# Optimization experiments

Hardware: AMD Instinct MI355X
Metric: run time of the kernel (lower is better)

The kernel has to match this reference:

```python
import jax, jax.numpy as jnp
import numpy as np

NEG_INF = -1000000000.0
B, S, E, H = 2, 2048, 1024, 16
HD = E // H


def setup_inputs() -> dict:
    key = jax.random.key(0)
    ks = jax.random.split(key, 5)
    sd = 1.0 / np.sqrt(E)
    return {
        "x": jax.random.normal(ks[0], (B, S, E), dtype=jnp.float32),
        "Wqkv": jax.random.normal(ks[1], (3 * E, E), dtype=jnp.float32) * sd,
        "bqkv": jax.random.normal(ks[2], (3 * E,), dtype=jnp.float32) * sd,
        "Wout": jax.random.normal(ks[3], (E, E), dtype=jnp.float32) * sd,
        "bout": jax.random.normal(ks[4], (E,), dtype=jnp.float32) * sd,
    }


def reference(x, Wqkv, bqkv, Wout, bout):
    # qkv projection (torch Linear: x @ W.T + b)
    qkv = x @ Wqkv.T + bqkv                      # [B, S, 3E]
    qkv = qkv.reshape(B, S, H, 3 * HD).transpose(0, 2, 1, 3)  # [B, H, S, 3*hd]
    q, k, v = jnp.split(qkv, 3, axis=-1)          # each [B, H, S, hd]
    scaled = jnp.einsum('bhqd,bhkd->bhqk', q, k) / jnp.sqrt(jnp.float32(HD))
    # faithful to source: mask = tril(ones) * NEG_INF (lower triangle incl. diagonal gets -1e9)
    mask = jnp.tril(jnp.ones((S, S), dtype=jnp.float32)) * NEG_INF
    scaled = scaled + mask                        # broadcast over [B, H]
    attention = jax.nn.softmax(scaled, axis=-1)
    values = jnp.einsum('bhqk,bhkd->bhqd', attention, v)
    values = values.transpose(0, 2, 1, 3).reshape(B, S, E)
    out = values @ Wout.T + bout
    return out
```

## Files before the change

### kernel.cpp

```cpp
#include <hip/hip_runtime.h>
#include <hip/hip_bf16.h>
#include <math.h>

#define Bb 2
#define Ss 2048
#define Ee 1024
#define Hh 16
#define HDd 64
#define NEG_INF_F -1000000000.0f

typedef __attribute__((ext_vector_type(8))) short bfrag;
typedef __attribute__((ext_vector_type(4))) float ffrag;
typedef __attribute__((ext_vector_type(16))) float ffrag16;
typedef __attribute__((ext_vector_type(8))) unsigned short us8;

#define C1F 0.1803368801f

#define WAIT_VM4 0x0F74
#define WAIT_VM0 0x0F70

__device__ __forceinline__ unsigned short f2bf(float x) {
  unsigned u = __float_as_uint(x);
  u += 0x7fffu + ((u >> 16) & 1u);
  return (unsigned short)(u >> 16);
}
__device__ __forceinline__ float bf2f(unsigned short h) {
  return __uint_as_float(((unsigned)h) << 16);
}

__device__ __forceinline__ void async_copy16(void* lds, const void* g) {
  __builtin_amdgcn_global_load_lds(
      (const __attribute__((address_space(1))) unsigned int*)g,
      (__attribute__((address_space(3))) unsigned int*)lds, 16, 0, 0);
}

__global__ __launch_bounds__(256) void split_all(
    const float* __restrict__ x, unsigned short* __restrict__ xh,
    const float* __restrict__ wq, unsigned short* __restrict__ wqh,
    unsigned short* __restrict__ wql,
    const float* __restrict__ wo, unsigned short* __restrict__ woh,
    unsigned short* __restrict__ wol) {
  int bid = blockIdx.x;
  const float* in;
  unsigned short *hi, *lo;
  if (bid < 4096) { in = x; hi = xh; lo = nullptr; }
  else if (bid < 7168) { bid -= 4096; in = wq; hi = wqh; lo = wql; }
  else { bid -= 7168; in = wo; hi = woh; lo = wol; }
  const int idx = (bid * 256 + threadIdx.x) * 4;
  const float4 v = *(const float4*)(in + idx);
  unsigned short h0 = f2bf(v.x), h1 = f2bf(v.y), h2 = f2bf(v.z), h3 = f2bf(v.w);
  ushort4 hv = {h0, h1, h2, h3};
  *(ushort4*)(hi + idx) = hv;
  if (lo) {
    ushort4 lv = {f2bf(v.x - bf2f(h0)), f2bf(v.y - bf2f(h1)),
                  f2bf(v.z - bf2f(h2)), f2bf(v.w - bf2f(h3))};
    *(ushort4*)(lo + idx) = lv;
  }
}

__device__ __forceinline__ int gemm_slot(int row, int q) {
  return (row >> 1) * 8 + ((((row & 1) * 4) | q) ^ ((row >> 1) & 7));
}
__device__ __forceinline__ int slot_src_off(int slot, int ld) {
  const int dr = slot >> 3;
  const int idx8 = (slot & 7) ^ (dr & 7);
  const int row = dr * 2 + (idx8 >> 2);
  const int q = idx8 & 3;
  return row * ld + q * 8;
}

__global__ __launch_bounds__(256) void gemm_qkv(
    const unsigned short* __restrict__ Ah,
    const unsigned short* __restrict__ Bh, const unsigned short* __restrict__ Bl,
    const float* __restrict__ bias,
    unsigned short* __restrict__ q_h, unsigned short* __restrict__ k_h,
    unsigned short* __restrict__ vt_h) {
  __shared__ unsigned short sm[3 * 4096];
  const int tid = threadIdx.x;
  const int lane = tid & 63;
  const int w = tid >> 6;
  const int wm = w >> 1;
  const int wn = w & 1;
  const int l31 = lane & 31;
  const int e = lane >> 5;
  const int m0 = blockIdx.x * 128;
  const int n0 = blockIdx.y * 128;

  int coff[2], ldsb[2];
#pragma unroll
  for (int u = 0; u < 2; ++u) {
    const int slot = w * 128 + u * 64 + lane;
    coff[u] = slot_src_off(slot, 1024);
    ldsb[u] = (w * 128 + u * 64) * 8;
  }
  const unsigned short* srcs[3] = {
      Ah + (size_t)m0 * 1024, Bh + (size_t)n0 * 1024, Bl + (size_t)n0 * 1024};

  ffrag16 acc[2][2];
#pragma unroll
  for (int i = 0; i < 2; ++i)
#pragma unroll
    for (int j = 0; j < 2; ++j) acc[i][j] = (ffrag16)0.f;

  int ca[2][2], cb[2][2];
#pragma unroll
  for (int t = 0; t < 2; ++t)
#pragma unroll
    for (int h2 = 0; h2 < 2; ++h2) {
      ca[t][h2] = gemm_slot(wm * 64 + t * 32 + l31, h2 * 2 + e) * 8;
      cb[t][h2] = gemm_slot(wn * 64 + t * 32 + l31, h2 * 2 + e) * 8;
    }

  for (int k0 = 0; k0 < 1024; k0 += 32) {
    __syncthreads();
#pragma unroll
    for (int t = 0; t < 3; ++t)
#pragma unroll
      for (int u = 0; u < 2; ++u)
        async_copy16(&sm[t * 4096 + ldsb[u]], srcs[t] + coff[u] + k0);
    __syncthreads();

    bfrag ah[2][2], bhf[2][2], blf[2][2];
#pragma unroll
    for (int t = 0; t < 2; ++t)
#pragma unroll
      for (int h2 = 0; h2 < 2; ++h2) {
        ah[t][h2] = *(const bfrag*)&sm[0 * 4096 + ca[t][h2]];
        bhf[t][h2] = *(const bfrag*)&sm[1 * 4096 + cb[t][h2]];
        blf[t][h2] = *(const bfrag*)&sm[2 * 4096 + cb[t][h2]];
      }
#pragma unroll
    for (int mt = 0; mt < 2; ++mt)
#pragma unroll
      for (int nt = 0; nt < 2; ++nt)
#pragma unroll
        for (int h2 = 0; h2 < 2; ++h2) {
          acc[mt][nt] = __builtin_amdgcn_mfma_f32_32x32x16_bf16(
              ah[mt][h2], bhf[nt][h2], acc[mt][nt], 0, 0, 0);
          acc[mt][nt] = __builtin_amdgcn_mfma_f32_32x32x16_bf16(
              ah[mt][h2], blf[nt][h2], acc[mt][nt], 0, 0, 0);
        }
  }

#pragma unroll
  for (int nt = 0; nt < 2; ++nt) {
    const int n = n0 + wn * 64 + nt * 32 + l31;
    const float bv = bias[n];
    const int h = n / 192;
    const int c = n - h * 192;
    const int d = c & 63;
#pragma unroll
    for (int mt = 0; mt < 2; ++mt) {
      if (c >= 128) {
#pragma unroll
        for (int g = 0; g < 4; ++g) {
          const int m = m0 + wm * 64 + mt * 32 + g * 8 + e * 4;
          const int bidx = m >> 11;
          const int s = m & 2047;
          ushort4 hv4;
          unsigned short* ph = (unsigned short*)&hv4;
#pragma unroll
          for (int r = 0; r < 4; ++r)
            ph[r] = f2bf(acc[mt][nt][g * 4 + r] + bv);
          const size_t off =
              (size_t)(bidx * 16 + h) * (64 * 2048) + (size_t)d * 2048 + s;
          *(ushort4*)(vt_h + off) = hv4;
        }
      } else {
        const float scale = (c < 64) ? C1F : 1.0f;
        unsigned short* dh = (c < 64) ? q_h : k_h;
#pragma unroll
        for (int g = 0; g < 4; ++g)
#pragma unroll
          for (int r = 0; r < 4; ++r) {
            const int m = m0 + wm * 64 + mt * 32 + g * 8 + e * 4 + r;
            const int bidx = m >> 11;
            const int s = m & 2047;
            const size_t off =
                (size_t)(bidx * 16 + h) * (2048 * 64) + (size_t)s * 64 + d;
            dh[off] = f2bf((acc[mt][nt][g * 4 + r] + bv) * scale);
          }
      }
    }
  }
}

__global__ __launch_bounds__(256) void gemm_out2(
    const unsigned short* __restrict__ A,
    const unsigned short* __restrict__ Bh, const unsigned short* __restrict__ Bl,
    const float* __restrict__ bias, float* __restrict__ out) {
  __shared__ unsigned short sm[8192];
  const int tid = threadIdx.x;
  const int lane = tid & 63;
  const int w = tid >> 6;
  const int wm = w >> 1;
  const int wn = w & 1;
  const int l31 = lane & 31;
  const int e = lane >> 5;
  const int m0 = blockIdx.x * 128;
  const int n0 = blockIdx.y * 64;

  int acoff[2], aldsb[2];
#pragma unroll
  for (int u = 0; u < 2; ++u) {
    const int slot = w * 128 + u * 64 + lane;
    acoff[u] = slot_src_off(slot, 1024);
    aldsb[u] = (w * 128 + u * 64) * 8;
  }
  const int bslot = w * 64 + lane;
  const int bcoff = slot_src_off(bslot, 1024);
  const int bldsb = bslot * 8;

  const unsigned short* Ap  = A + (size_t)m0 * 1024;
  const unsigned short* Bph = Bh + (size_t)n0 * 1024;
  const unsigned short* Bpl = Bl + (size_t)n0 * 1024;

  ffrag16 acc[2];
  acc[0] = (ffrag16)0.f;
  acc[1] = (ffrag16)0.f;

  int ca[2][2], cb[2];
#pragma unroll
  for (int t = 0; t < 2; ++t)
#pragma unroll
    for (int h2 = 0; h2 < 2; ++h2)
      ca[t][h2] = gemm_slot(wm * 64 + t * 32 + l31, h2 * 2 + e) * 8;
#pragma unroll
  for (int h2 = 0; h2 < 2; ++h2)
    cb[h2] = gemm_slot(wn * 32 + l31, h2 * 2 + e) * 8;

  for (int k0 = 0; k0 < 1024; k0 += 32) {
    __syncthreads();
#pragma unroll
    for (int u = 0; u < 2; ++u)
      async_copy16(&sm[0 + aldsb[u]], Ap + acoff[u] + k0);
    async_copy16(&sm[4096 + bldsb], Bph + bcoff + k0);
    async_copy16(&sm[6144 + bldsb], Bpl + bcoff + k0);
    __syncthreads();

    bfrag ah[2][2], bhf[2], blf[2];
#pragma unroll
    for (int t = 0; t < 2; ++t)
#pragma unroll
      for (int h2 = 0; h2 < 2; ++h2)
        ah[t][h2] = *(const bfrag*)&sm[0 + ca[t][h2]];
#pragma unroll
    for (int h2 = 0; h2 < 2; ++h2) {
      bhf[h2] = *(const bfrag*)&sm[4096 + cb[h2]];
      blf[h2] = *(const bfrag*)&sm[6144 + cb[h2]];
    }
#pragma unroll
    for (int mt = 0; mt < 2; ++mt)
#pragma unroll
      for (int h2 = 0; h2 < 2; ++h2) {
        acc[mt] = __builtin_amdgcn_mfma_f32_32x32x16_bf16(
            ah[mt][h2], bhf[h2], acc[mt], 0, 0, 0);
        acc[mt] = __builtin_amdgcn_mfma_f32_32x32x16_bf16(
            ah[mt][h2], blf[h2], acc[mt], 0, 0, 0);
      }
  }

  const int n = n0 + wn * 32 + l31;
  const float bv = bias[n];
#pragma unroll
  for (int mt = 0; mt < 2; ++mt)
#pragma unroll
    for (int g = 0; g < 4; ++g)
#pragma unroll
      for (int r = 0; r < 4; ++r) {
        const int m = m0 + wm * 64 + mt * 32 + g * 8 + e * 4 + r;
        out[(size_t)m * 1024 + n] = acc[mt][g * 4 + r] + bv;
      }
}

__global__ __launch_bounds__(256) void attn_pair(
    const unsigned short* __restrict__ qh, const unsigned short* __restrict__ kh,
    const unsigned short* __restrict__ vth, unsigned short* __restrict__ vals) {
  __shared__ unsigned short sm[3 * 8192 + 8192];
  const int tid = threadIdx.x;
  const int lane = tid & 63;
  const int w = tid >> 6;
  const int l15 = lane & 15;
  const int quad = lane >> 4;
  const int bh = blockIdx.x;
  const int y = blockIdx.y;
  const int rbase[2] = {64 * y + 16 * w, 64 * (31 - y) + 16 * w};
  const int ktB = 31 - y;
  const bool fix = (y == 0) && (w == 3);
  const size_t base = (size_t)bh * (Ss * HDd);
  const int PB = 24576;

  bfrag Qh[2][2];
#pragma unroll
  for (int mt = 0; mt < 2; ++mt)
#pragma unroll
    for (int ks = 0; ks < 2; ++ks) {
      const size_t off = base + (size_t)(rbase[mt] + l15) * 64 + ks * 32 + quad * 8;
      Qh[mt][ks] = *(const bfrag*)(qh + off);
    }

  bfrag vone;
#pragma unroll
  for (int j = 0; j < 8; ++j) vone[j] = (short)0x3F80;

  const int c0 = w * 128 + lane;
  const int c1 = c0 + 64;
  const int r0 = c0 >> 3, r1 = c1 >> 3;
  const int s0 = ((c0 & 7) ^ (r0 & 7)) * 8;
  const int s1 = ((c1 & 7) ^ (r1 & 7)) * 8;
  const int koff0 = r0 * 64 + s0, koff1 = r1 * 64 + s1;
  const int voff0 = r0 * 2048 + s0, voff1 = r1 * 2048 + s1;
  const int ldsc0 = (w * 128) * 8;
  const int ldsc1 = (w * 128 + 64) * 8;

  ffrag O[2][4], Oe[2], Vsum[4];
#pragma unroll
  for (int mt = 0; mt < 2; ++mt) {
#pragma unroll
    for (int dt = 0; dt < 4; ++dt) O[mt][dt] = (ffrag)0.f;
    Oe[mt] = (ffrag)0.f;
  }
#pragma unroll
  for (int dt = 0; dt < 4; ++dt) Vsum[dt] = (ffrag)0.f;

  {
    const unsigned short* kph = kh + base + y * 4096;
    const unsigned short* vph = vth + base + y * 64;
    async_copy16(&sm[0 + ldsc0], kph + koff0);
    async_copy16(&sm[0 + ldsc1], kph + koff1);
    async_copy16(&sm[4096 + ldsc0], vph + voff0);
    async_copy16(&sm[4096 + ldsc1], vph + voff1);
    const unsigned short* kph1 = kh + base + (y + 1) * 4096;
    const unsigned short* vph1 = vth + base + (y + 1) * 64;
    async_copy16(&sm[8192 + 0 + ldsc0], kph1 + koff0);
    async_copy16(&sm[8192 + 0 + ldsc1], kph1 + koff1);
    async_copy16(&sm[8192 + 4096 + ldsc0], vph1 + voff0);
    async_copy16(&sm[8192 + 4096 + ldsc1], vph1 + voff1);
  }

  int b0 = 0, b1 = 8192, b2 = 16384;
  for (int kt = y; kt < 32; ++kt) {
    if (kt + 1 < 32) __builtin_amdgcn_s_waitcnt(WAIT_VM4);
    else             __builtin_amdgcn_s_waitcnt(WAIT_VM0);
    __builtin_amdgcn_s_barrier();
    __builtin_amdgcn_sched_barrier(0);
    if (kt + 2 < 32) {
      const unsigned short* kph = kh + base + (kt + 2) * 4096;
      const unsigned short* vph = vth + base + (kt + 2) * 64;
      async_copy16(&sm[b2 + 0 + ldsc0], kph + koff0);
      async_copy16(&sm[b2 + 0 + ldsc1], kph + koff1);
      async_copy16(&sm[b2 + 4096 + ldsc0], vph + voff0);
      async_copy16(&sm[b2 + 4096 + ldsc1], vph + voff1);
    }
    const bool bact = (kt >= ktB);

    ffrag S[2][4];
#pragma unroll
    for (int mt = 0; mt < 2; ++mt)
#pragma unroll
      for (int nt = 0; nt < 4; ++nt) S[mt][nt] = (ffrag)0.f;
#pragma unroll
    for (int nt = 0; nt < 4; ++nt) {
      const int krow = nt * 16 + l15;
#pragma unroll
      for (int ks = 0; ks < 2; ++ks) {
        const int koffr = b0 + krow * 64 + ((ks * 4 + quad) ^ (krow & 7)) * 8;
        const bfrag kbh = *(const bfrag*)&sm[koffr];
        S[0][nt] = __builtin_amdgcn_mfma_f32_16x16x32_bf16(Qh[0][ks], kbh, S[0][nt], 0, 0, 0);
        if (bact)
          S[1][nt] = __builtin_amdgcn_mfma_f32_16x16x32_bf16(Qh[1][ks], kbh, S[1][nt], 0, 0, 0);
      }
    }

    const float CM = -1.442695041e9f;
#pragma unroll
    for (int mt = 0; mt < 2; ++mt) {
      if (mt == 1 && !bact) continue;
      const bool partial = (kt == (mt == 0 ? y : ktB));
#pragma unroll
      for (int nt = 0; nt < 4; ++nt) {
        const int key = nt * 16 + l15;
#pragma unroll
        for (int rp = 0; rp < 2; ++rp) {
          float t0 = S[mt][nt][2 * rp];
          float t1 = S[mt][nt][2 * rp + 1];
          if (partial) {
            const int jg = kt * 64 + key;
            const int ig = rbase[mt] + quad * 4 + 2 * rp;
            if (jg <= ig) t0 += CM;
            if (jg <= ig + 1) t1 += CM;
          }
          float2 pf;
          pf.x = __builtin_amdgcn_exp2f(t0);
          pf.y = __builtin_amdgcn_exp2f(t1);
          const __hip_bfloat162 pb = __float22bfloat162_rn(pf);
          const unsigned short* pbs = (const unsigned short*)&pb;
          const int prow0 = w * 32 + mt * 16 + quad * 4 + 2 * rp;
          sm[PB + prow0 * 64 + (((key >> 3) ^ (prow0 & 7)) * 8 + (key & 7))] = pbs[0];
          const int prow1 = prow0 + 1;
          sm[PB + prow1 * 64 + (((key >> 3) ^ (prow1 & 7)) * 8 + (key & 7))] = pbs[1];
        }
      }
    }

#pragma unroll
    for (int ks = 0; ks < 2; ++ks) {
      bfrag pA[2];
#pragma unroll
      for (int mt = 0; mt < 2; ++mt) {
        if (mt == 1 && !bact) continue;
        const int prow = w * 32 + mt * 16 + l15;
        pA[mt] = *(const bfrag*)&sm[PB + prow * 64 + ((ks * 4 + quad) ^ (prow & 7)) * 8];
      }
      Oe[0] = __builtin_amdgcn_mfma_f32_16x16x32_bf16(pA[0], vone, Oe[0], 0, 0, 0);
      if (bact)
        Oe[1] = __builtin_amdgcn_mfma_f32_16x16x32_bf16(pA[1], vone, Oe[1], 0, 0, 0);
#pragma unroll
      for (int dt = 0; dt < 4; ++dt) {
        const int vrow = dt * 16 + l15;
        const int voffr = b0 + 4096 + vrow * 64 + ((ks * 4 + quad) ^ (vrow & 7)) * 8;
        const bfrag vbh = *(const bfrag*)&sm[voffr];
        O[0][dt] = __builtin_amdgcn_mfma_f32_16x16x32_bf16(pA[0], vbh, O[0][dt], 0, 0, 0);
        if (bact)
          O[1][dt] = __builtin_amdgcn_mfma_f32_16x16x32_bf16(pA[1], vbh, O[1][dt], 0, 0, 0);
        if (fix)
          Vsum[dt] = __builtin_amdgcn_mfma_f32_16x16x32_bf16(vone, vbh, Vsum[dt], 0, 0, 0);
      }
    }
    const int t = b0; b0 = b1; b1 = b2; b2 = t;
  }

  const int b = bh >> 4;
  const int h = bh & 15;
#pragma unroll
  for (int mt = 0; mt < 2; ++mt)
#pragma unroll
    for (int r = 0; r < 4; ++r) {
      const float inv = 1.0f / Oe[mt][r];
      const int s = rbase[mt] + quad * 4 + r;
      const size_t rowoff = ((size_t)b * 2048 + s) * 1024 + h * 64;
#pragma unroll
      for (int dt = 0; dt < 4; ++dt) {
        float val = O[mt][dt][r] * inv;
        if (fix && mt == 1 && quad == 3 && r == 3)
          val = Vsum[dt][r] * (1.0f / 2048.0f);
        vals[rowoff + dt * 16 + l15] = f2bf(val);
      }
    }
}

extern "C" void kernel_launch(void* const* d_in, const int* in_sizes, int n_in,
                              void* d_out, int out_size, void* d_ws, size_t ws_size,
                              hipStream_t stream) {
  const float* x    = (const float*)d_in[0];
  const float* Wqkv = (const float*)d_in[1];
  const float* bqkv = (const float*)d_in[2];
  const float* Wout = (const float*)d_in[3];
  const float* bout = (const float*)d_in[4];
  float* out = (float*)d_out;
  char* wsb = (char*)d_ws;

  unsigned short* qhp  = (unsigned short*)d_ws;
  unsigned short* khp  = qhp + 1 * 4194304;
  unsigned short* vthp = qhp + 2 * 4194304;
  unsigned short* vals = qhp + 3 * 4194304;
  unsigned short* wqh  = (unsigned short*)(wsb + (48u << 20));
  unsigned short* wql  = (unsigned short*)(wsb + (54u << 20));
  unsigned short* woh  = (unsigned short*)(wsb + (60u << 20));
  unsigned short* wol  = (unsigned short*)(wsb + (62u << 20));
  unsigned short* xh   = (unsigned short*)d_out;

  dim3 blk(256);
  split_all<<<8192, blk, 0, stream>>>(x, xh, Wqkv, wqh, wql, Wout, woh, wol);
  gemm_qkv<<<dim3(32, 24), blk, 0, stream>>>(xh, wqh, wql, bqkv, qhp, khp, vthp);
  attn_pair<<<dim3(32, 16), blk, 0, stream>>>(qhp, khp, vthp, vals);
  gemm_out2<<<dim3(32, 16), blk, 0, stream>>>(vals, woh, wol, bout, out);
}
```

Measured before the change: 224.7 us.

## Split paired attention rows across 8 independent waves with direct global K/V loads

The attention kernel moves from 256 threads, each wave handling two row tiles (front and mirrored back) with a triple-buffered LDS async-copy pipeline, to 512 threads where waves 0-3 take the front tile and waves 4-7 take the back tile. The shared K/V staging and block barriers are gone: each wave reads K and V fragments straight from global memory (through cache) into MFMA operands. Only per-wave P tiles stay in LDS. This removes barrier coupling and the divergence from the bact predicates and raises occupancy. The cost is redundant global/L2 traffic, since each wave now loads K/V separately, and transposed-V loads that are strided across 2048-element rows.

```diff
diff --git a/kernel.cpp b/kernel.cpp
--- a/kernel.cpp
+++ b/kernel.cpp
@@ -15,9 +15,6 @@
 typedef __attribute__((ext_vector_type(8))) unsigned short us8;
 
 #define C1F 0.1803368801f
-
-#define WAIT_VM4 0x0F74
-#define WAIT_VM0 0x0F70
 
 __device__ __forceinline__ unsigned short f2bf(float x) {
   unsigned u = __float_as_uint(x);
@@ -273,180 +270,120 @@
       }
 }
 
-__global__ __launch_bounds__(256) void attn_pair(
+__global__ __launch_bounds__(512, 4) void attn_ws(
     const unsigned short* __restrict__ qh, const unsigned short* __restrict__ kh,
     const unsigned short* __restrict__ vth, unsigned short* __restrict__ vals) {
-  __shared__ unsigned short sm[3 * 8192 + 8192];
+  __shared__ unsigned short smP[8 * 16 * 64];
   const int tid = threadIdx.x;
   const int lane = tid & 63;
   const int w = tid >> 6;
+  const int wi = w & 3;
+  const bool isB = (w >= 4);
   const int l15 = lane & 15;
   const int quad = lane >> 4;
   const int bh = blockIdx.x;
   const int y = blockIdx.y;
-  const int rbase[2] = {64 * y + 16 * w, 64 * (31 - y) + 16 * w};
-  const int ktB = 31 - y;
-  const bool fix = (y == 0) && (w == 3);
+  const int yb = isB ? (31 - y) : y;
+  const int rb = 64 * yb + 16 * wi;
+  const int kt0 = yb;
   const size_t base = (size_t)bh * (Ss * HDd);
-  const int PB = 24576;
-
-  bfrag Qh[2][2];
-#pragma unroll
-  for (int mt = 0; mt < 2; ++mt)
+  const bool fixsrc = (y == 0) && (w == 3);
+  const bool fixskip = (y == 0) && (w == 7);
+
+  bfrag Qf[2];
+#pragma unroll
+  for (int ks = 0; ks < 2; ++ks)
+    Qf[ks] = *(const bfrag*)(qh + base + (size_t)(rb + l15) * 64 + ks * 32 + quad * 8);
+
+  bfrag vone;
+#pragma unroll
+  for (int j = 0; j < 8; ++j) vone[j] = (short)0x3F80;
+
+  ffrag O[4], Oe, Vsum[4];
+#pragma unroll
+  for (int dt = 0; dt < 4; ++dt) { O[dt] = (ffrag)0.f; Vsum[dt] = (ffrag)0.f; }
+  Oe = (ffrag)0.f;
+
+  const int pbase = w * (16 * 64);
+
+  for (int kt = kt0; kt < 32; ++kt) {
+    const bool partial = (kt == kt0);
+
+    ffrag S[4];
+#pragma unroll
+    for (int nt = 0; nt < 4; ++nt) S[nt] = (ffrag)0.f;
+#pragma unroll
+    for (int nt = 0; nt < 4; ++nt) {
+      const int krow = kt * 64 + nt * 16 + l15;
+#pragma unroll
+      for (int ks = 0; ks < 2; ++ks) {
+        const bfrag kbh =
+            *(const bfrag*)(kh + base + (size_t)krow * 64 + ks * 32 + quad * 8);
+        S[nt] = __builtin_amdgcn_mfma_f32_16x16x32_bf16(Qf[ks], kbh, S[nt], 0, 0, 0);
+      }
+    }
+
+    const float CM = -1.442695041e9f;
+#pragma unroll
+    for (int nt = 0; nt < 4; ++nt) {
+      const int key = nt * 16 + l15;
+#pragma unroll
+      for (int rp = 0; rp < 2; ++rp) {
+        float t0 = S[nt][2 * rp];
+        float t1 = S[nt][2 * rp + 1];
+        if (partial) {
+          const int jg = kt * 64 + key;
+          const int ig = rb + quad * 4 + 2 * rp;
+          if (jg <= ig) t0 += CM;
+          if (jg <= ig + 1) t1 += CM;
+        }
+        float2 pf;
+        pf.x = __builtin_amdgcn_exp2f(t0);
+        pf.y = __builtin_amdgcn_exp2f(t1);
+        const __hip_bfloat162 pb = __float22bfloat162_rn(pf);
+        const unsigned short* pbs = (const unsigned short*)&pb;
+        const int pr0 = quad * 4 + 2 * rp;
+        smP[pbase + pr0 * 64 + (((key >> 3) ^ (pr0 & 7)) * 8 + (key & 7))] = pbs[0];
+        const int pr1 = pr0 + 1;
+        smP[pbase + pr1 * 64 + (((key >> 3) ^ (pr1 & 7)) * 8 + (key & 7))] = pbs[1];
+      }
+    }
+
 #pragma unroll
     for (int ks = 0; ks < 2; ++ks) {
-      const size_t off = base + (size_t)(rbase[mt] + l15) * 64 + ks * 32 + quad * 8;
-      Qh[mt][ks] = *(const bfrag*)(qh + off);
-    }
-
-  bfrag vone;
-#pragma unroll
-  for (int j = 0; j < 8; ++j) vone[j] = (short)0x3F80;
-
-  const int c0 = w * 128 + lane;
-  const int c1 = c0 + 64;
-  const int r0 = c0 >> 3, r1 = c1 >> 3;
-  const int s0 = ((c0 & 7) ^ (r0 & 7)) * 8;
-  const int s1 = ((c1 & 7) ^ (r1 & 7)) * 8;
-  const int koff0 = r0 * 64 + s0, koff1 = r1 * 64 + s1;
-  const int voff0 = r0 * 2048 + s0, voff1 = r1 * 2048 + s1;
-  const int ldsc0 = (w * 128) * 8;
-  const int ldsc1 = (w * 128 + 64) * 8;
-
-  ffrag O[2][4], Oe[2], Vsum[4];
-#pragma unroll
-  for (int mt = 0; mt < 2; ++mt) {
-#pragma unroll
-    for (int dt = 0; dt < 4; ++dt) O[mt][dt] = (ffrag)0.f;
-    Oe[mt] = (ffrag)0.f;
-  }
-#pragma unroll
-  for (int dt = 0; dt < 4; ++dt) Vsum[dt] = (ffrag)0.f;
-
-  {
-    const unsigned short* kph = kh + base + y * 4096;
-    const unsigned short* vph = vth + base + y * 64;
-    async_copy16(&sm[0 + ldsc0], kph + koff0);
-    async_copy16(&sm[0 + ldsc1], kph + koff1);
-    async_copy16(&sm[4096 + ldsc0], vph + voff0);
-    async_copy16(&sm[4096 + ldsc1], vph + voff1);
-    const unsigned short* kph1 = kh + base + (y + 1) * 4096;
-    const unsigned short* vph1 = vth + base + (y + 1) * 64;
-    async_copy16(&sm[8192 + 0 + ldsc0], kph1 + koff0);
-    async_copy16(&sm[8192 + 0 + ldsc1], kph1 + koff1);
-    async_copy16(&sm[8192 + 4096 + ldsc0], vph1 + voff0);
-    async_copy16(&sm[8192 + 4096 + ldsc1], vph1 + voff1);
-  }
-
-  int b0 = 0, b1 = 8192, b2 = 16384;
-  for (int kt = y; kt < 32; ++kt) {
-    if (kt + 1 < 32) __builtin_amdgcn_s_waitcnt(WAIT_VM4);
-    else             __builtin_amdgcn_s_waitcnt(WAIT_VM0);
-    __builtin_amdgcn_s_barrier();
-    __builtin_amdgcn_sched_barrier(0);
-    if (kt + 2 < 32) {
-      const unsigned short* kph = kh + base + (kt + 2) * 4096;
-      const unsigned short* vph = vth + base + (kt + 2) * 64;
-      async_copy16(&sm[b2 + 0 + ldsc0], kph + koff0);
-      async_copy16(&sm[b2 + 0 + ldsc1], kph + koff1);
-      async_copy16(&sm[b2 + 4096 + ldsc0], vph + voff0);
-      async_copy16(&sm[b2 + 4096 + ldsc1], vph + voff1);
-    }
-    const bool bact = (kt >= ktB);
-
-    ffrag S[2][4];
-#pragma unroll
-    for (int mt = 0; mt < 2; ++mt)
-#pragma unroll
-      for (int nt = 0; nt < 4; ++nt) S[mt][nt] = (ffrag)0.f;
-#pragma unroll
-    for (int nt = 0; nt < 4; ++nt) {
-      const int krow = nt * 16 + l15;
-#pragma unroll
-      for (int ks = 0; ks < 2; ++ks) {
-        const int koffr = b0 + krow * 64 + ((ks * 4 + quad) ^ (krow & 7)) * 8;
-        const bfrag kbh = *(const bfrag*)&sm[koffr];
-        S[0][nt] = __builtin_amdgcn_mfma_f32_16x16x32_bf16(Qh[0][ks], kbh, S[0][nt], 0, 0, 0);
-        if (bact)
-          S[1][nt] = __builtin_amdgcn_mfma_f32_16x16x32_bf16(Qh[1][ks], kbh, S[1][nt], 0, 0, 0);
-      }
-    }
-
-    const float CM = -1.442695041e9f;
-#pragma unroll
-    for (int mt = 0; mt < 2; ++mt) {
-      if (mt == 1 && !bact) continue;
-      const bool partial = (kt == (mt == 0 ? y : ktB));
-#pragma unroll
-      for (int nt = 0; nt < 4; ++nt) {
-        const int key = nt * 16 + l15;
-#pragma unroll
-        for (int rp = 0; rp < 2; ++rp) {
-          float t0 = S[mt][nt][2 * rp];
-          float t1 = S[mt][nt][2 * rp + 1];
-          if (partial) {
-            const int jg = kt * 64 + key;
-            const int ig = rbase[mt] + quad * 4 + 2 * rp;
-            if (jg <= ig) t0 += CM;
-            if (jg <= ig + 1) t1 += CM;
-          }
-          float2 pf;
-          pf.x = __builtin_amdgcn_exp2f(t0);
-          pf.y = __builtin_amdgcn_exp2f(t1);
-          const __hip_bfloat162 pb = __float22bfloat162_rn(pf);
-          const unsigned short* pbs = (const unsigned short*)&pb;
-          const int prow0 = w * 32 + mt * 16 + quad * 4 + 2 * rp;
-          sm[PB + prow0 * 64 + (((key >> 3) ^ (prow0 & 7)) * 8 + (key & 7))] = pbs[0];
-          const int prow1 = prow0 + 1;
-          sm[PB + prow1 * 64 + (((key >> 3) ^ (prow1 & 7)) * 8 + (key & 7))] = pbs[1];
-        }
-      }
-    }
-
-#pragma unroll
-    for (int ks = 0; ks < 2; ++ks) {
-      bfrag pA[2];
-#pragma unroll
-      for (int mt = 0; mt < 2; ++mt) {
-        if (mt == 1 && !bact) continue;
-        const int prow = w * 32 + mt * 16 + l15;
-        pA[mt] = *(const bfrag*)&sm[PB + prow * 64 + ((ks * 4 + quad) ^ (prow & 7)) * 8];
-      }
-      Oe[0] = __builtin_amdgcn_mfma_f32_16x16x32_bf16(pA[0], vone, Oe[0], 0, 0, 0);
-      if (bact)
-        Oe[1] = __builtin_amdgcn_mfma_f32_16x16x32_bf16(pA[1], vone, Oe[1], 0, 0, 0);
+      const bfrag pA =
+          *(const bfrag*)&smP[pbase + l15 * 64 + (((ks * 4 + quad) ^ (l15 & 7)) * 8)];
+      Oe = __builtin_amdgcn_mfma_f32_16x16x32_bf16(pA, vone, Oe, 0, 0, 0);
 #pragma unroll
       for (int dt = 0; dt < 4; ++dt) {
-        const int vrow = dt * 16 + l15;
-        const int voffr = b0 + 4096 + vrow * 64 + ((ks * 4 + quad) ^ (vrow & 7)) * 8;
-        const bfrag vbh = *(const bfrag*)&sm[voffr];
-        O[0][dt] = __builtin_amdgcn_mfma_f32_16x16x32_bf16(pA[0], vbh, O[0][dt], 0, 0, 0);
-        if (bact)
-          O[1][dt] = __builtin_amdgcn_mfma_f32_16x16x32_bf16(pA[1], vbh, O[1][dt], 0, 0, 0);
-        if (fix)
+        const bfrag vbh = *(const bfrag*)(vth + base + (size_t)(dt * 16 + l15) * 2048 +
+                                          kt * 64 + ks * 32 + quad * 8);
+        O[dt] = __builtin_amdgcn_mfma_f32_16x16x32_bf16(pA, vbh, O[dt], 0, 0, 0);
+        if (fixsrc)
           Vsum[dt] = __builtin_amdgcn_mfma_f32_16x16x32_bf16(vone, vbh, Vsum[dt], 0, 0, 0);
       }
     }
-    const int t = b0; b0 = b1; b1 = b2; b2 = t;
   }
 
   const int b = bh >> 4;
   const int h = bh & 15;
 #pragma unroll
-  for (int mt = 0; mt < 2; ++mt)
-#pragma unroll
-    for (int r = 0; r < 4; ++r) {
-      const float inv = 1.0f / Oe[mt][r];
-      const int s = rbase[mt] + quad * 4 + r;
-      const size_t rowoff = ((size_t)b * 2048 + s) * 1024 + h * 64;
-#pragma unroll
-      for (int dt = 0; dt < 4; ++dt) {
-        float val = O[mt][dt][r] * inv;
-        if (fix && mt == 1 && quad == 3 && r == 3)
-          val = Vsum[dt][r] * (1.0f / 2048.0f);
-        vals[rowoff + dt * 16 + l15] = f2bf(val);
-      }
-    }
+  for (int r = 0; r < 4; ++r) {
+    const float inv = 1.0f / Oe[r];
+    const int s = rb + quad * 4 + r;
+    const size_t rowoff = ((size_t)b * 2048 + s) * 1024 + h * 64;
+#pragma unroll
+    for (int dt = 0; dt < 4; ++dt) {
+      if (fixskip && s == 2047) continue;
+      vals[rowoff + dt * 16 + l15] = f2bf(O[dt][r] * inv);
+    }
+  }
+  if (fixsrc && quad == 3) {
+    const size_t rowoff = ((size_t)b * 2048 + 2047) * 1024 + h * 64;
+#pragma unroll
+    for (int dt = 0; dt < 4; ++dt)
+      vals[rowoff + dt * 16 + l15] = f2bf(Vsum[dt][3] * (1.0f / 2048.0f));
+  }
 }
 
 extern "C" void kernel_launch(void* const* d_in, const int* in_sizes, int n_in,
@@ -473,6 +410,6 @@
   dim3 blk(256);
   split_all<<<8192, blk, 0, stream>>>(x, xh, Wqkv, wqh, wql, Wout, woh, wol);
   gemm_qkv<<<dim3(32, 24), blk, 0, stream>>>(xh, wqh, wql, bqkv, qhp, khp, vthp);
-  attn_pair<<<dim3(32, 16), blk, 0, stream>>>(qhp, khp, vthp, vals);
+  attn_ws<<<dim3(32, 16), dim3(512), 0, stream>>>(qhp, khp, vthp, vals);
   gemm_out2<<<dim3(32, 16), blk, 0, stream>>>(vals, woh, wol, bout, out);
 }
```

After: 282.6 us. 1.26x slower.

## Load K/V tiles directly from global into registers, dropping the LDS triple buffer

Applied to the files above, without the earlier changes.

The attention kernel no longer stages K and V tiles through a triple-buffered LDS pipeline with async copies and barriers. Each wave now reads its K and V fragments straight from global memory into registers every iteration, and LDS is kept only for the P tile. A launch-bounds occupancy hint of 4 blocks is added. This removes the barriers and the LDS traffic, but every wave redundantly fetches the same K/V from global/L2 without prefetch, which risks exposing memory latency.

```diff
diff --git a/kernel.cpp b/kernel.cpp
--- a/kernel.cpp
+++ b/kernel.cpp
@@ -15,9 +15,6 @@
 typedef __attribute__((ext_vector_type(8))) unsigned short us8;
 
 #define C1F 0.1803368801f
-
-#define WAIT_VM4 0x0F74
-#define WAIT_VM0 0x0F70
 
 __device__ __forceinline__ unsigned short f2bf(float x) {
   unsigned u = __float_as_uint(x);
@@ -273,10 +270,10 @@
       }
 }
 
-__global__ __launch_bounds__(256) void attn_pair(
+__global__ __launch_bounds__(256, 4) void attn_dg(
     const unsigned short* __restrict__ qh, const unsigned short* __restrict__ kh,
     const unsigned short* __restrict__ vth, unsigned short* __restrict__ vals) {
-  __shared__ unsigned short sm[3 * 8192 + 8192];
+  __shared__ unsigned short smP[4 * 32 * 64];
   const int tid = threadIdx.x;
   const int lane = tid & 63;
   const int w = tid >> 6;
@@ -288,7 +285,6 @@
   const int ktB = 31 - y;
   const bool fix = (y == 0) && (w == 3);
   const size_t base = (size_t)bh * (Ss * HDd);
-  const int PB = 24576;
 
   bfrag Qh[2][2];
 #pragma unroll
@@ -303,16 +299,6 @@
 #pragma unroll
   for (int j = 0; j < 8; ++j) vone[j] = (short)0x3F80;
 
-  const int c0 = w * 128 + lane;
-  const int c1 = c0 + 64;
-  const int r0 = c0 >> 3, r1 = c1 >> 3;
-  const int s0 = ((c0 & 7) ^ (r0 & 7)) * 8;
-  const int s1 = ((c1 & 7) ^ (r1 & 7)) * 8;
-  const int koff0 = r0 * 64 + s0, koff1 = r1 * 64 + s1;
-  const int voff0 = r0 * 2048 + s0, voff1 = r1 * 2048 + s1;
-  const int ldsc0 = (w * 128) * 8;
-  const int ldsc1 = (w * 128 + 64) * 8;
-
   ffrag O[2][4], Oe[2], Vsum[4];
 #pragma unroll
   for (int mt = 0; mt < 2; ++mt) {
@@ -323,54 +309,41 @@
 #pragma unroll
   for (int dt = 0; dt < 4; ++dt) Vsum[dt] = (ffrag)0.f;
 
-  {
-    const unsigned short* kph = kh + base + y * 4096;
-    const unsigned short* vph = vth + base + y * 64;
-    async_copy16(&sm[0 + ldsc0], kph + koff0);
-    async_copy16(&sm[0 + ldsc1], kph + koff1);
-    async_copy16(&sm[4096 + ldsc0], vph + voff0);
-    async_copy16(&sm[4096 + ldsc1], vph + voff1);
-    const unsigned short* kph1 = kh + base + (y + 1) * 4096;
-    const unsigned short* vph1 = vth + base + (y + 1) * 64;
-    async_copy16(&sm[8192 + 0 + ldsc0], kph1 + koff0);
-    async_copy16(&sm[8192 + 0 + ldsc1], kph1 + koff1);
-    async_copy16(&sm[8192 + 4096 + ldsc0], vph1 + voff0);
-    async_copy16(&sm[8192 + 4096 + ldsc1], vph1 + voff1);
-  }
-
-  int b0 = 0, b1 = 8192, b2 = 16384;
   for (int kt = y; kt < 32; ++kt) {
-    if (kt + 1 < 32) __builtin_amdgcn_s_waitcnt(WAIT_VM4);
-    else             __builtin_amdgcn_s_waitcnt(WAIT_VM0);
-    __builtin_amdgcn_s_barrier();
-    __builtin_amdgcn_sched_barrier(0);
-    if (kt + 2 < 32) {
-      const unsigned short* kph = kh + base + (kt + 2) * 4096;
-      const unsigned short* vph = vth + base + (kt + 2) * 64;
-      async_copy16(&sm[b2 + 0 + ldsc0], kph + koff0);
-      async_copy16(&sm[b2 + 0 + ldsc1], kph + koff1);
-      async_copy16(&sm[b2 + 4096 + ldsc0], vph + voff0);
-      async_copy16(&sm[b2 + 4096 + ldsc1], vph + voff1);
-    }
     const bool bact = (kt >= ktB);
 
+    bfrag Kreg[4][2];
+#pragma unroll
+    for (int nt = 0; nt < 4; ++nt) {
+      const int krow = kt * 64 + nt * 16 + l15;
+#pragma unroll
+      for (int ks = 0; ks < 2; ++ks)
+        Kreg[nt][ks] =
+            *(const bfrag*)(kh + base + (size_t)krow * 64 + ks * 32 + quad * 8);
+    }
     ffrag S[2][4];
 #pragma unroll
     for (int mt = 0; mt < 2; ++mt)
 #pragma unroll
       for (int nt = 0; nt < 4; ++nt) S[mt][nt] = (ffrag)0.f;
 #pragma unroll
-    for (int nt = 0; nt < 4; ++nt) {
-      const int krow = nt * 16 + l15;
+    for (int nt = 0; nt < 4; ++nt)
 #pragma unroll
       for (int ks = 0; ks < 2; ++ks) {
-        const int koffr = b0 + krow * 64 + ((ks * 4 + quad) ^ (krow & 7)) * 8;
-        const bfrag kbh = *(const bfrag*)&sm[koffr];
-        S[0][nt] = __builtin_amdgcn_mfma_f32_16x16x32_bf16(Qh[0][ks], kbh, S[0][nt], 0, 0, 0);
+        S[0][nt] = __builtin_amdgcn_mfma_f32_16x16x32_bf16(Qh[0][ks], Kreg[nt][ks],
+                                                           S[0][nt], 0, 0, 0);
         if (bact)
-          S[1][nt] = __builtin_amdgcn_mfma_f32_16x16x32_bf16(Qh[1][ks], kbh, S[1][nt], 0, 0, 0);
-      }
-    }
+          S[1][nt] = __builtin_amdgcn_mfma_f32_16x16x32_bf16(Qh[1][ks], Kreg[nt][ks],
+                                                             S[1][nt], 0, 0, 0);
+      }
+
+    bfrag Vreg[2][4];
+#pragma unroll
+    for (int ks = 0; ks < 2; ++ks)
+#pragma unroll
+      for (int dt = 0; dt < 4; ++dt)
+        Vreg[ks][dt] = *(const bfrag*)(vth + base + (size_t)(dt * 16 + l15) * 2048 +
+                                       kt * 64 + ks * 32 + quad * 8);
 
     const float CM = -1.442695041e9f;
 #pragma unroll
@@ -396,9 +369,9 @@
           const __hip_bfloat162 pb = __float22bfloat162_rn(pf);
           const unsigned short* pbs = (const unsigned short*)&pb;
           const int prow0 = w * 32 + mt * 16 + quad * 4 + 2 * rp;
-          sm[PB + prow0 * 64 + (((key >> 3) ^ (prow0 & 7)) * 8 + (key & 7))] = pbs[0];
+          smP[prow0 * 64 + (((key >> 3) ^ (prow0 & 7)) * 8 + (key & 7))] = pbs[0];
           const int prow1 = prow0 + 1;
-          sm[PB + prow1 * 64 + (((key >> 3) ^ (prow1 & 7)) * 8 + (key & 7))] = pbs[1];
+          smP[prow1 * 64 + (((key >> 3) ^ (prow1 & 7)) * 8 + (key & 7))] = pbs[1];
         }
       }
     }
@@ -410,24 +383,23 @@
       for (int mt = 0; mt < 2; ++mt) {
         if (mt == 1 && !bact) continue;
         const int prow = w * 32 + mt * 16 + l15;
-        pA[mt] = *(const bfrag*)&sm[PB + prow * 64 + ((ks * 4 + quad) ^ (prow & 7)) * 8];
+        pA[mt] = *(const bfrag*)&smP[prow * 64 + ((ks * 4 + quad) ^ (prow & 7)) * 8];
       }
       Oe[0] = __builtin_amdgcn_mfma_f32_16x16x32_bf16(pA[0], vone, Oe[0], 0, 0, 0);
       if (bact)
         Oe[1] = __builtin_amdgcn_mfma_f32_16x16x32_bf16(pA[1], vone, Oe[1], 0, 0, 0);
 #pragma unroll
       for (int dt = 0; dt < 4; ++dt) {
-        const int vrow = dt * 16 + l15;
-        const int voffr = b0 + 4096 + vrow * 64 + ((ks * 4 + quad) ^ (vrow & 7)) * 8;
-        const bfrag vbh = *(const bfrag*)&sm[voffr];
-        O[0][dt] = __builtin_amdgcn_mfma_f32_16x16x32_bf16(pA[0], vbh, O[0][dt], 0, 0, 0);
+        O[0][dt] = __builtin_amdgcn_mfma_f32_16x16x32_bf16(pA[0], Vreg[ks][dt],
+                                                           O[0][dt], 0, 0, 0);
         if (bact)
-          O[1][dt] = __builtin_amdgcn_mfma_f32_16x16x32_bf16(pA[1], vbh, O[1][dt], 0, 0, 0);
+          O[1][dt] = __builtin_amdgcn_mfma_f32_16x16x32_bf16(pA[1], Vreg[ks][dt],
+                                                             O[1][dt], 0, 0, 0);
         if (fix)
-          Vsum[dt] = __builtin_amdgcn_mfma_f32_16x16x32_bf16(vone, vbh, Vsum[dt], 0, 0, 0);
-      }
-    }
-    const int t = b0; b0 = b1; b1 = b2; b2 = t;
+          Vsum[dt] = __builtin_amdgcn_mfma_f32_16x16x32_bf16(vone, Vreg[ks][dt],
+                                                             Vsum[dt], 0, 0, 0);
+      }
+    }
   }
 
   const int b = bh >> 4;
@@ -473,6 +445,6 @@
   dim3 blk(256);
   split_all<<<8192, blk, 0, stream>>>(x, xh, Wqkv, wqh, wql, Wout, woh, wol);
   gemm_qkv<<<dim3(32, 24), blk, 0, stream>>>(xh, wqh, wql, bqkv, qhp, khp, vthp);
-  attn_pair<<<dim3(32, 16), blk, 0, stream>>>(qhp, khp, vthp, vals);
+  attn_dg<<<dim3(32, 16), blk, 0, stream>>>(qhp, khp, vthp, vals);
   gemm_out2<<<dim3(32, 16), blk, 0, stream>>>(vals, woh, wol, bout, out);
 }
```

Measured after the change: 422.4 us. 1.88x slower.
